# Kernel optimization log

Hardware: AMD Instinct MI355X
Metric: run time of the kernel (lower is better)

The kernel has to match this reference:

```python
import math
import jax, jax.numpy as jnp
import numpy as np

B, L, D, H = 4, 4096, 1024, 16
DK = D // H


def setup_inputs() -> dict:
    key = jax.random.key(0)
    ks = jax.random.split(key, 11)
    s = 0.02
    return {
        "queries": jax.random.normal(ks[0], (B, L, D), jnp.float32),
        "keys": jax.random.normal(ks[1], (B, L, D), jnp.float32),
        "values": jax.random.normal(ks[2], (B, L, D), jnp.float32),
        "Wq": jax.random.normal(ks[3], (D, D), jnp.float32) * s,
        "bq": jnp.zeros((D,), jnp.float32),
        "Wk": jax.random.normal(ks[4], (D, D), jnp.float32) * s,
        "bk": jnp.zeros((D,), jnp.float32),
        "Wv": jax.random.normal(ks[5], (D, D), jnp.float32) * s,
        "bv": jnp.zeros((D,), jnp.float32),
        "Wo": jax.random.normal(ks[6], (D, D), jnp.float32) * s,
        "bo": jnp.zeros((D,), jnp.float32),
    }


def reference(queries, keys, values, Wq, bq, Wk, bk, Wv, bv, Wo, bo):
    # projections + split heads: (B, H, L, DK)
    q = (queries @ Wq + bq).reshape(B, L, H, DK).transpose(0, 2, 1, 3)
    k = (keys @ Wk + bk).reshape(B, L, H, DK).transpose(0, 2, 1, 3)
    v = (values @ Wv + bv).reshape(B, L, H, DK).transpose(0, 2, 1, 3)

    # per-head mean over channel dim -> (B, H, L)
    qm = q.mean(axis=-1)
    km = k.mean(axis=-1)

    # FFT-based autocorrelation: corr (B, H, L)
    qf = jnp.fft.rfft(qm, axis=-1)
    kf = jnp.fft.rfft(km, axis=-1)
    corr = jnp.fft.irfft(qf * jnp.conj(kf), n=L, axis=-1)

    top_k = max(1, int(math.log(L)))  # top_k=None path -> 8 for L=4096
    w, delays = jax.lax.top_k(corr, top_k)          # (B, H, K)
    w = jax.nn.softmax(w, axis=-1)

    # torch.roll(x, shift=d): out[i] = x[(i - d) mod L]
    pos = jnp.arange(L)
    out = jnp.zeros_like(v)
    for kk in range(top_k):
        idx = (pos[None, None, :] - delays[:, :, kk, None]) % L  # (B, H, L)
        rolled = jnp.take_along_axis(v, idx[..., None], axis=2)  # (B, H, L, DK)
        out = out + w[:, :, kk, None, None] * rolled

    # merge heads (matches per-head concat order) and output projection
    out = out.transpose(0, 2, 1, 3).reshape(B, L, D)
    return out @ Wo + bo
```

## Files before the change

kernel.cpp:

```cpp
#include <hip/hip_runtime.h>
#include <hip/hip_bf16.h>
#include <cstdint>

#define BB 4
#define LL 4096
#define DD 1024
#define HH 16
#define DKH 64
#define MROWS 16384
#define KTOP 8
#define RPB 16

typedef float f32x4 __attribute__((ext_vector_type(4)));
typedef _Float16 f16;
typedef _Float16 f16x4 __attribute__((ext_vector_type(4)));
typedef _Float16 f16x8 __attribute__((ext_vector_type(8)));

__device__ __forceinline__ void gll16(const void* g, void* l) {
    __builtin_amdgcn_global_load_lds(
        (const __attribute__((address_space(1))) void*)g,
        (__attribute__((address_space(3))) void*)l, 16, 0, 0);
}

template <int CTRL>
__device__ __forceinline__ float dppf(float x) {
    return __builtin_bit_cast(float,
        __builtin_amdgcn_update_dpp(0, __builtin_bit_cast(int, x), CTRL, 0xF, 0xF, true));
}

__global__ void k_colmeans(const float* __restrict__ Wq, const float* __restrict__ bq,
                           const float* __restrict__ Wk, const float* __restrict__ bk,
                           float* __restrict__ Wqm_t, float* __restrict__ Wkm_t,
                           float* __restrict__ bqm, float* __restrict__ bkm) {
    int t = blockIdx.x * blockDim.x + threadIdx.x;
    int which = t >> 14;
    int idx = t & 16383;
    int d = idx >> 4;
    int h = idx & 15;
    const float* W = which ? Wk : Wq;
    const float* p = W + d * DD + h * DKH;
    float s = 0.f;
    #pragma unroll
    for (int c = 0; c < DKH; ++c) s += p[c];
    (which ? Wkm_t : Wqm_t)[h * DD + d] = s * (1.0f / DKH);
    if (d == 0) {
        const float* bb = which ? bk : bq;
        float sb = 0.f;
        for (int c = 0; c < DKH; ++c) sb += bb[h * DKH + c];
        (which ? bkm : bqm)[h] = sb * (1.0f / DKH);
    }
}

__global__ void k_transpose_cvt(const float* __restrict__ in, f16* __restrict__ out) {
    __shared__ float tile[32][33];
    int k0 = blockIdx.x * 32;
    int n0 = blockIdx.y * 32;
    int tx = threadIdx.x, ty = threadIdx.y;
    #pragma unroll
    for (int j = 0; j < 32; j += 8)
        tile[ty + j][tx] = in[(k0 + ty + j) * DD + n0 + tx];
    __syncthreads();
    #pragma unroll
    for (int j = 0; j < 32; j += 8)
        out[(n0 + ty + j) * DD + k0 + tx] = (f16)tile[tx][ty + j];
}

__global__ void k_cvt_f16(const float* __restrict__ in, f16* __restrict__ out) {
    int i = blockIdx.x * blockDim.x + threadIdx.x;
    f32x4 v = ((const f32x4*)in)[i];
    f16x4 o;
    o[0] = (f16)v.x; o[1] = (f16)v.y; o[2] = (f16)v.z; o[3] = (f16)v.w;
    ((f16x4*)out)[i] = o;
}

__global__ __launch_bounds__(256, 4) void k_means(const float* __restrict__ q, const float* __restrict__ k,
                        const float* __restrict__ Wqm_t, const float* __restrict__ Wkm_t,
                        const float* __restrict__ bqm, const float* __restrict__ bkm,
                        float* __restrict__ qm, float* __restrict__ km) {
    __shared__ float lred[RPB * 264];
    int isK = blockIdx.x & 1;
    int rb  = blockIdx.x >> 1;
    const float* src = isK ? k : q;
    const float* W   = isK ? Wkm_t : Wqm_t;
    const float* bm  = isK ? bkm : bqm;
    float* dst = isK ? km : qm;
    int t = threadIdx.x;
    int wavei = t >> 6, lane = t & 63;
    int c = wavei * 256 + lane * 4;
    f32x4 wr[16];
    #pragma unroll
    for (int h = 0; h < 16; ++h) wr[h] = *(const f32x4*)(W + h * DD + c);
    #pragma unroll
    for (int h = 0; h < 16; ++h) asm volatile("" : "+v"(wr[h]));
    const float* rbase = src + (size_t)rb * RPB * DD + c;
    f32x4 rv = *(const f32x4*)rbase;
    #pragma unroll
    for (int r = 0; r < RPB; ++r) {
        f32x4 nxt = rv;
        if (r + 1 < RPB) nxt = *(const f32x4*)(rbase + (r + 1) * DD);
        float v[16];
        #pragma unroll
        for (int h = 0; h < 16; ++h)
            v[h] = rv.x * wr[h].x + rv.y * wr[h].y + rv.z * wr[h].z + rv.w * wr[h].w;
        float u[8];
        #pragma unroll
        for (int i = 0; i < 8; ++i) {
            float keep = (lane & 1) ? v[2*i+1] : v[2*i];
            float send = (lane & 1) ? v[2*i]   : v[2*i+1];
            u[i] = keep + dppf<0xB1>(send);
        }
        float w2[4];
        #pragma unroll
        for (int i = 0; i < 4; ++i) {
            float keep = (lane & 2) ? u[2*i+1] : u[2*i];
            float send = (lane & 2) ? u[2*i]   : u[2*i+1];
            w2[i] = keep + dppf<0x4E>(send);
        }
        float y[2];
        #pragma unroll
        for (int i = 0; i < 2; ++i) {
            float keep = (lane & 8) ? w2[2*i+1] : w2[2*i];
            float send = (lane & 8) ? w2[2*i]   : w2[2*i+1];
            y[i] = keep + dppf<0x128>(send);
        }
        {
            float keep = (lane & 4) ? y[1] : y[0];
            float send = (lane & 4) ? y[0] : y[1];
            float z = keep + __shfl_xor(send, 4);
            lred[r * 264 + wavei * 64 + lane] = z;
        }
        rv = nxt;
    }
    __syncthreads();
    int rr = t >> 4, h = t & 15;
    int lp = (h & 3) | (((h >> 2) & 1) << 3) | (((h >> 3) & 1) << 2);
    float s = bm[h];
    #pragma unroll
    for (int w = 0; w < 4; ++w)
        #pragma unroll
        for (int g = 0; g < 4; ++g)
            s += lred[rr * 264 + w * 64 + g * 16 + lp];
    int row = rb * RPB + rr;
    int b = row >> 12, l = row & 4095;
    dst[((size_t)((b << 4) + h) << 12) + l] = s;
}

__global__ __launch_bounds__(1024) void k_corr(const float* __restrict__ qm,
                                               const float* __restrict__ km,
                                               float* __restrict__ corr) {
    __shared__ float sq[LL];
    __shared__ f32x4 red[1024];
    int bh = blockIdx.x >> 2;
    int lag0 = (blockIdx.x & 3) * 1024;
    const f32x4* qg = (const f32x4*)(qm + bh * LL);
    const f32x4* kg = (const f32x4*)(km + bh * LL);
    f32x4* sq4 = (f32x4*)sq;
    int t = threadIdx.x;
    for (int i = t; i < LL / 4; i += 1024) sq4[i] = qg[i];
    __syncthreads();
    int lt = t & 255;
    int ms = t >> 8;
    int d0 = lag0 + lt * 4;
    int m0 = ms * 1024;
    float a0 = 0, a1 = 0, a2 = 0, a3 = 0;
    f32x4 wv = sq4[((m0 + d0) & 4095) >> 2];
    float w0 = wv.x, w1 = wv.y, w2 = wv.z, w3 = wv.w;
    #pragma unroll 4
    for (int m = m0; m < m0 + 1024; m += 4) {
        f32x4 nx = sq4[((m + 4 + d0) & 4095) >> 2];
        int mi = __builtin_amdgcn_readfirstlane(m >> 2);
        f32x4 kv = kg[mi];
        a0 += kv.x * w0;  a1 += kv.x * w1;  a2 += kv.x * w2;  a3 += kv.x * w3;
        a0 += kv.y * w1;  a1 += kv.y * w2;  a2 += kv.y * w3;  a3 += kv.y * nx.x;
        a0 += kv.z * w2;  a1 += kv.z * w3;  a2 += kv.z * nx.x; a3 += kv.z * nx.y;
        a0 += kv.w * w3;  a1 += kv.w * nx.x; a2 += kv.w * nx.y; a3 += kv.w * nx.z;
        w0 = nx.x; w1 = nx.y; w2 = nx.z; w3 = nx.w;
    }
    f32x4 p; p.x = a0; p.y = a1; p.z = a2; p.w = a3;
    red[t] = p;
    __syncthreads();
    if (t < 256) {
        f32x4 s0 = red[t], s1 = red[256 + t], s2 = red[512 + t], s3 = red[768 + t];
        f32x4 s;
        s.x = s0.x + s1.x + s2.x + s3.x;
        s.y = s0.y + s1.y + s2.y + s3.y;
        s.z = s0.z + s1.z + s2.z + s3.z;
        s.w = s0.w + s1.w + s2.w + s3.w;
        *(f32x4*)(corr + bh * LL + lag0 + t * 4) = s;
    }
}

__global__ __launch_bounds__(256) void k_topk(const float* __restrict__ corr,
                                              float* __restrict__ wts, int* __restrict__ dls) {
    __shared__ float sc[LL];
    __shared__ float rv[4]; __shared__ int ri[4];
    __shared__ float topv[KTOP]; __shared__ int topi[KTOP];
    int bh = blockIdx.x;
    for (int i = threadIdx.x; i < LL; i += 256) sc[i] = corr[bh * LL + i];
    for (int kk = 0; kk < KTOP; ++kk) {
        __syncthreads();
        float bv = -1e30f; int bi = 0;
        for (int i = threadIdx.x; i < LL; i += 256) {
            float v = sc[i];
            if (v > bv) { bv = v; bi = i; }
        }
        #pragma unroll
        for (int off = 32; off; off >>= 1) {
            float ov = __shfl_down(bv, off);
            int oi = __shfl_down(bi, off);
            if (ov > bv || (ov == bv && oi < bi)) { bv = ov; bi = oi; }
        }
        int wid = threadIdx.x >> 6;
        if ((threadIdx.x & 63) == 0) { rv[wid] = bv; ri[wid] = bi; }
        __syncthreads();
        if (threadIdx.x == 0) {
            for (int w = 1; w < 4; ++w)
                if (rv[w] > bv || (rv[w] == bv && ri[w] < bi)) { bv = rv[w]; bi = ri[w]; }
            topv[kk] = bv; topi[kk] = bi;
            sc[bi] = -1e30f;
        }
    }
    __syncthreads();
    if (threadIdx.x == 0) {
        float mx = topv[0], s = 0.f, e[KTOP];
        #pragma unroll
        for (int kk = 0; kk < KTOP; ++kk) { e[kk] = __expf(topv[kk] - mx); s += e[kk]; }
        float inv = 1.0f / s;
        #pragma unroll
        for (int kk = 0; kk < KTOP; ++kk) {
            wts[bh * KTOP + kk] = e[kk] * inv;
            dls[bh * KTOP + kk] = topi[kk];
        }
    }
}

#define BM 128
#define BN 128
#define BKK 32
template <int MODE>
__global__ __launch_bounds__(256) void k_gemm_bt(const f16* __restrict__ A,
                                                 const f16* __restrict__ BT,
                                                 const float* __restrict__ bias,
                                                 void* __restrict__ Cout) {
    __shared__ f16 As[2][BM * BKK];
    __shared__ f16 Bs[2][BN * BKK];
    const int K = DD;
    int m0 = blockIdx.x * BM;
    int n0 = blockIdx.y * BN;
    int tid = threadIdx.x;
    int lane = tid & 63;
    int wave = tid >> 6;
    int wm = wave & 1, wn = wave >> 1;

    int row0 = tid >> 2;
    int slot = tid & 3;
    int kc0 = slot ^ ((row0 >> 1) & 3);
    int row1 = row0 + 64;
    int kc1 = slot ^ ((row1 >> 1) & 3);
    const f16* gA0 = A + (size_t)(m0 + row0) * K + kc0 * 8;
    const f16* gA1 = A + (size_t)(m0 + row1) * K + kc1 * 8;
    const f16* gB0 = BT + (size_t)(n0 + row0) * K + kc0 * 8;
    const f16* gB1 = BT + (size_t)(n0 + row1) * K + kc1 * 8;

    int fr = lane & 15;
    int quad = lane >> 4;
    int a_off[4], b_off[4];
    #pragma unroll
    for (int i = 0; i < 4; ++i) {
        int ra = wm * 64 + i * 16 + fr;
        a_off[i] = (ra * 4 + (quad ^ ((ra >> 1) & 3))) * 8;
        int rb = wn * 64 + i * 16 + fr;
        b_off[i] = (rb * 4 + (quad ^ ((rb >> 1) & 3))) * 8;
    }

    f32x4 acc[4][4] = {};

    auto STAGE = [&](int b) {
        char* la = (char*)As + b * 8192 + wave * 1024;
        char* lb = (char*)Bs + b * 8192 + wave * 1024;
        gll16(gA0, la);
        gll16(gA1, la + 4096);
        gll16(gB0, lb);
        gll16(gB1, lb + 4096);
        gA0 += BKK; gA1 += BKK; gB0 += BKK; gB1 += BKK;
    };
    auto COMPUTE = [&](int b) {
        const f16* Ab = As[b];
        const f16* Bb = Bs[b];
        f16x8 af[4], bf[4];
        #pragma unroll
        for (int i = 0; i < 4; ++i) af[i] = *(const f16x8*)(Ab + a_off[i]);
        #pragma unroll
        for (int i = 0; i < 4; ++i) bf[i] = *(const f16x8*)(Bb + b_off[i]);
        #pragma unroll
        for (int im = 0; im < 4; ++im)
            #pragma unroll
            for (int in = 0; in < 4; ++in)
                acc[im][in] = __builtin_amdgcn_mfma_f32_16x16x32_f16(af[im], bf[in], acc[im][in], 0, 0, 0);
    };

    STAGE(0);
    __syncthreads();
    const int NT = K / BKK;
    for (int kt = 0; kt < NT - 1; ++kt) {
        STAGE((kt & 1) ^ 1);
        COMPUTE(kt & 1);
        __syncthreads();
    }
    COMPUTE((NT - 1) & 1);

    #pragma unroll
    for (int in = 0; in < 4; ++in) {
        int col = n0 + wn * 64 + in * 16 + fr;
        float bb = bias[col];
        #pragma unroll
        for (int im = 0; im < 4; ++im) {
            int rowb = m0 + wm * 64 + im * 16 + quad * 4;
            #pragma unroll
            for (int r = 0; r < 4; ++r) {
                float val = acc[im][in][r] + bb;
                if (MODE == 0) {
                    int rr = rowb + r;
                    int b = rr >> 12, l = rr & 4095, h = col >> 6, c = col & 63;
                    ((f16*)Cout)[((size_t)(((b << 4) + h) << 12) + l) * 64 + c] = (f16)val;
                } else {
                    ((float*)Cout)[(size_t)(rowb + r) * DD + col] = val;
                }
            }
        }
    }
}

__global__ __launch_bounds__(256) void k_roll(const f16* __restrict__ V,
                                              const float* __restrict__ wts,
                                              const int* __restrict__ dls,
                                              f16* __restrict__ out) {
    int x = blockIdx.x;
    int wk = ((x & 7) << 10) | (x >> 3);
    int t = wk * 256 + threadIdx.x;
    int cc = t & 7;
    int l = (t >> 3) & 4095;
    int bh = t >> 15;
    const f16* vb = V + ((size_t)bh << 18);
    float a[8] = {};
    #pragma unroll
    for (int kk = 0; kk < KTOP; ++kk) {
        float w = wts[bh * KTOP + kk];
        int d = dls[bh * KTOP + kk];
        int src = (l - d) & 4095;
        f16x8 vv = *(const f16x8*)(vb + (src << 6) + (cc << 3));
        #pragma unroll
        for (int j = 0; j < 8; ++j) a[j] += w * (float)vv[j];
    }
    f16* o = out + ((size_t)((bh >> 4) << 12) + l) * 1024 + ((bh & 15) << 6) + (cc << 3);
    f16x8 ov;
    #pragma unroll
    for (int j = 0; j < 8; ++j) ov[j] = (f16)a[j];
    *(f16x8*)o = ov;
}

extern "C" void kernel_launch(void* const* d_in, const int* in_sizes, int n_in,
                              void* d_out, int out_size, void* d_ws, size_t ws_size,
                              hipStream_t stream) {
    const float* queries = (const float*)d_in[0];
    const float* keys    = (const float*)d_in[1];
    const float* values  = (const float*)d_in[2];
    const float* Wq = (const float*)d_in[3];
    const float* bq = (const float*)d_in[4];
    const float* Wk = (const float*)d_in[5];
    const float* bk = (const float*)d_in[6];
    const float* Wv = (const float*)d_in[7];
    const float* bv = (const float*)d_in[8];
    const float* Wo = (const float*)d_in[9];
    const float* bo = (const float*)d_in[10];

    char* ws = (char*)d_ws;
    size_t off = 0;
    auto alloc = [&](size_t bytes) -> char* {
        char* p = ws + off;
        off += (bytes + 255) & ~(size_t)255;
        return p;
    };
    f16*   values_f16 = (f16*)alloc((size_t)MROWS * DD * 2);
    f16*   Vbuf       = (f16*)alloc((size_t)MROWS * DD * 2);
    f16*   WvT        = (f16*)alloc((size_t)DD * DD * 2);
    f16*   WoT        = (f16*)alloc((size_t)DD * DD * 2);
    float* Wqm_t      = (float*)alloc(HH * DD * 4);
    float* Wkm_t      = (float*)alloc(HH * DD * 4);
    float* bqm        = (float*)alloc(HH * 4);
    float* bkm        = (float*)alloc(HH * 4);
    float* qm         = (float*)alloc((size_t)BB * HH * LL * 4);
    float* km         = (float*)alloc((size_t)BB * HH * LL * 4);
    float* corr       = (float*)alloc((size_t)BB * HH * LL * 4);
    float* wts        = (float*)alloc(BB * HH * KTOP * 4);
    int*   dls        = (int*)alloc(BB * HH * KTOP * 4);
    f16*   out_f16    = values_f16;

    k_colmeans<<<128, 256, 0, stream>>>(Wq, bq, Wk, bk, Wqm_t, Wkm_t, bqm, bkm);
    k_transpose_cvt<<<dim3(32, 32), dim3(32, 8), 0, stream>>>(Wv, WvT);
    k_transpose_cvt<<<dim3(32, 32), dim3(32, 8), 0, stream>>>(Wo, WoT);
    k_cvt_f16<<<16384, 256, 0, stream>>>(values, values_f16);
    k_means<<<2048, 256, 0, stream>>>(queries, keys, Wqm_t, Wkm_t, bqm, bkm, qm, km);
    k_corr<<<256, 1024, 0, stream>>>(qm, km, corr);
    k_topk<<<64, 256, 0, stream>>>(corr, wts, dls);
    k_gemm_bt<0><<<dim3(MROWS / BM, DD / BN), 256, 0, stream>>>(values_f16, WvT, bv, Vbuf);
    k_roll<<<8192, 256, 0, stream>>>(Vbuf, wts, dls, out_f16);
    k_gemm_bt<1><<<dim3(MROWS / BM, DD / BN), 256, 0, stream>>>(out_f16, WoT, bo, d_out);
}
```

Baseline: 449.0 us.

## Triple-buffer GEMM LDS tiles with explicit vmcnt waits and raw barriers

Expands the GEMM shared-memory staging from two to three buffers so two K-tiles are in flight while one is computed. The loop is unrolled by three, with `s_waitcnt vmcnt(4)` plus `s_barrier` replacing `__syncthreads`. Only the current tile's async global-to-LDS loads are awaited, which keeps more memory latency hidden behind MFMA work. In exchange, LDS per block rises to 48KB, which can lower occupancy, and correctness now depends on hand-counted outstanding loads.

```diff
diff --git a/kernel.cpp b/kernel.cpp
--- a/kernel.cpp
+++ b/kernel.cpp
@@ -242,8 +242,8 @@
                                                  const f16* __restrict__ BT,
                                                  const float* __restrict__ bias,
                                                  void* __restrict__ Cout) {
-    __shared__ f16 As[2][BM * BKK];
-    __shared__ f16 Bs[2][BN * BKK];
+    __shared__ f16 As[3][BM * BKK];
+    __shared__ f16 Bs[3][BN * BKK];
     const int K = DD;
     int m0 = blockIdx.x * BM;
     int n0 = blockIdx.y * BN;
@@ -275,18 +275,18 @@
 
     f32x4 acc[4][4] = {};
 
-    auto STAGE = [&](int b) {
-        char* la = (char*)As + b * 8192 + wave * 1024;
-        char* lb = (char*)Bs + b * 8192 + wave * 1024;
-        gll16(gA0, la);
-        gll16(gA1, la + 4096);
-        gll16(gB0, lb);
-        gll16(gB1, lb + 4096);
-        gA0 += BKK; gA1 += BKK; gB0 += BKK; gB1 += BKK;
+    auto STAGE = [&](int b, int kt) {
+        char* la = (char*)(&As[b][0]) + wave * 1024;
+        char* lb = (char*)(&Bs[b][0]) + wave * 1024;
+        int ko = kt * BKK;
+        gll16(gA0 + ko, la);
+        gll16(gA1 + ko, la + 4096);
+        gll16(gB0 + ko, lb);
+        gll16(gB1 + ko, lb + 4096);
     };
     auto COMPUTE = [&](int b) {
-        const f16* Ab = As[b];
-        const f16* Bb = Bs[b];
+        const f16* Ab = &As[b][0];
+        const f16* Bb = &Bs[b][0];
         f16x8 af[4], bf[4];
         #pragma unroll
         for (int i = 0; i < 4; ++i) af[i] = *(const f16x8*)(Ab + a_off[i]);
@@ -299,15 +299,29 @@
                 acc[im][in] = __builtin_amdgcn_mfma_f32_16x16x32_f16(af[im], bf[in], acc[im][in], 0, 0, 0);
     };
 
-    STAGE(0);
-    __syncthreads();
     const int NT = K / BKK;
-    for (int kt = 0; kt < NT - 1; ++kt) {
-        STAGE((kt & 1) ^ 1);
-        COMPUTE(kt & 1);
-        __syncthreads();
-    }
-    COMPUTE((NT - 1) & 1);
+    STAGE(0, 0);
+    STAGE(1, 1);
+    for (int ii = 0; ii < NT - 2; ii += 3) {
+        asm volatile("s_waitcnt vmcnt(4)" ::: "memory");
+        __builtin_amdgcn_s_barrier();
+        STAGE(2, ii + 2);
+        COMPUTE(0);
+        asm volatile("s_waitcnt vmcnt(4)" ::: "memory");
+        __builtin_amdgcn_s_barrier();
+        STAGE(0, ii + 3);
+        COMPUTE(1);
+        asm volatile("s_waitcnt vmcnt(4)" ::: "memory");
+        __builtin_amdgcn_s_barrier();
+        STAGE(1, ii + 4);
+        COMPUTE(2);
+    }
+    asm volatile("s_waitcnt vmcnt(4)" ::: "memory");
+    __builtin_amdgcn_s_barrier();
+    COMPUTE(0);
+    asm volatile("s_waitcnt vmcnt(0)" ::: "memory");
+    __builtin_amdgcn_s_barrier();
+    COMPUTE(1);
 
     #pragma unroll
     for (int in = 0; in < 4; ++in) {
```

New measurement: 437.2 us. 2.6% less time.

## Enlarge GEMM M-tile, load B fragments directly from global, widen corr key loads

Applied to the files above, without the earlier changes.

The GEMM now uses a 256x128 tile. B operand fragments are loaded straight from global memory into registers instead of being staged through LDS, so LDS holds only the A tile. The main loop is unrolled by two with explicit register double-buffering. The correlation kernel loads 16 keys per wavefront-uniform load with one-group prefetch, cutting the number of scalar loads. This should improve MFMA arithmetic intensity and halve LDS traffic per FLOP, but it raises register pressure and relies on uncoalesced per-lane global loads for B.

```diff
diff --git a/kernel.cpp b/kernel.cpp
--- a/kernel.cpp
+++ b/kernel.cpp
@@ -12,6 +12,7 @@
 #define RPB 16
 
 typedef float f32x4 __attribute__((ext_vector_type(4)));
+typedef float f32x16 __attribute__((ext_vector_type(16)));
 typedef _Float16 f16;
 typedef _Float16 f16x4 __attribute__((ext_vector_type(4)));
 typedef _Float16 f16x8 __attribute__((ext_vector_type(8)));
@@ -153,7 +154,7 @@
     int bh = blockIdx.x >> 2;
     int lag0 = (blockIdx.x & 3) * 1024;
     const f32x4* qg = (const f32x4*)(qm + bh * LL);
-    const f32x4* kg = (const f32x4*)(km + bh * LL);
+    const f32x16* kg16 = (const f32x16*)(km + bh * LL);
     f32x4* sq4 = (f32x4*)sq;
     int t = threadIdx.x;
     for (int i = t; i < LL / 4; i += 1024) sq4[i] = qg[i];
@@ -162,19 +163,26 @@
     int ms = t >> 8;
     int d0 = lag0 + lt * 4;
     int m0 = ms * 1024;
+    int gi0 = m0 >> 4;
     float a0 = 0, a1 = 0, a2 = 0, a3 = 0;
     f32x4 wv = sq4[((m0 + d0) & 4095) >> 2];
     float w0 = wv.x, w1 = wv.y, w2 = wv.z, w3 = wv.w;
-    #pragma unroll 4
-    for (int m = m0; m < m0 + 1024; m += 4) {
-        f32x4 nx = sq4[((m + 4 + d0) & 4095) >> 2];
-        int mi = __builtin_amdgcn_readfirstlane(m >> 2);
-        f32x4 kv = kg[mi];
-        a0 += kv.x * w0;  a1 += kv.x * w1;  a2 += kv.x * w2;  a3 += kv.x * w3;
-        a0 += kv.y * w1;  a1 += kv.y * w2;  a2 += kv.y * w3;  a3 += kv.y * nx.x;
-        a0 += kv.z * w2;  a1 += kv.z * w3;  a2 += kv.z * nx.x; a3 += kv.z * nx.y;
-        a0 += kv.w * w3;  a1 += kv.w * nx.x; a2 += kv.w * nx.y; a3 += kv.w * nx.z;
-        w0 = nx.x; w1 = nx.y; w2 = nx.z; w3 = nx.w;
+    f32x16 kv = kg16[__builtin_amdgcn_readfirstlane(gi0)];
+    for (int g = 0; g < 64; ++g) {
+        f32x16 kvn = kv;
+        if (g < 63) kvn = kg16[__builtin_amdgcn_readfirstlane(gi0 + g + 1)];
+        #pragma unroll
+        for (int j = 0; j < 4; ++j) {
+            int m = m0 + g * 16 + j * 4;
+            f32x4 nx = sq4[((m + 4 + d0) & 4095) >> 2];
+            float kx = kv[4*j+0], ky = kv[4*j+1], kz = kv[4*j+2], kw = kv[4*j+3];
+            a0 += kx * w0;  a1 += kx * w1;  a2 += kx * w2;  a3 += kx * w3;
+            a0 += ky * w1;  a1 += ky * w2;  a2 += ky * w3;  a3 += ky * nx.x;
+            a0 += kz * w2;  a1 += kz * w3;  a2 += kz * nx.x; a3 += kz * nx.y;
+            a0 += kw * w3;  a1 += kw * nx.x; a2 += kw * nx.y; a3 += kw * nx.z;
+            w0 = nx.x; w1 = nx.y; w2 = nx.z; w3 = nx.w;
+        }
+        kv = kvn;
     }
     f32x4 p; p.x = a0; p.y = a1; p.z = a2; p.w = a3;
     red[t] = p;
@@ -234,16 +242,15 @@
     }
 }
 
-#define BM 128
+#define BM 256
 #define BN 128
 #define BKK 32
 template <int MODE>
-__global__ __launch_bounds__(256) void k_gemm_bt(const f16* __restrict__ A,
-                                                 const f16* __restrict__ BT,
-                                                 const float* __restrict__ bias,
-                                                 void* __restrict__ Cout) {
+__global__ __launch_bounds__(256, 2) void k_gemm_bt(const f16* __restrict__ A,
+                                                    const f16* __restrict__ BT,
+                                                    const float* __restrict__ bias,
+                                                    void* __restrict__ Cout) {
     __shared__ f16 As[2][BM * BKK];
-    __shared__ f16 Bs[2][BN * BKK];
     const int K = DD;
     int m0 = blockIdx.x * BM;
     int n0 = blockIdx.y * BN;
@@ -252,70 +259,82 @@
     int wave = tid >> 6;
     int wm = wave & 1, wn = wave >> 1;
 
-    int row0 = tid >> 2;
+    int rowS = tid >> 2;
     int slot = tid & 3;
-    int kc0 = slot ^ ((row0 >> 1) & 3);
-    int row1 = row0 + 64;
-    int kc1 = slot ^ ((row1 >> 1) & 3);
-    const f16* gA0 = A + (size_t)(m0 + row0) * K + kc0 * 8;
-    const f16* gA1 = A + (size_t)(m0 + row1) * K + kc1 * 8;
-    const f16* gB0 = BT + (size_t)(n0 + row0) * K + kc0 * 8;
-    const f16* gB1 = BT + (size_t)(n0 + row1) * K + kc1 * 8;
+    int kcS = slot ^ ((rowS >> 1) & 3);
+    const f16* gA0 = A + (size_t)(m0 + rowS) * K + kcS * 8;
+    const f16* gA1 = A + (size_t)(m0 + rowS + 64) * K + kcS * 8;
+    const f16* gA2 = A + (size_t)(m0 + rowS + 128) * K + kcS * 8;
+    const f16* gA3 = A + (size_t)(m0 + rowS + 192) * K + kcS * 8;
 
     int fr = lane & 15;
     int quad = lane >> 4;
-    int a_off[4], b_off[4];
-    #pragma unroll
-    for (int i = 0; i < 4; ++i) {
-        int ra = wm * 64 + i * 16 + fr;
+    int a_off[8];
+    #pragma unroll
+    for (int i = 0; i < 8; ++i) {
+        int ra = wm * 128 + i * 16 + fr;
         a_off[i] = (ra * 4 + (quad ^ ((ra >> 1) & 3))) * 8;
-        int rb = wn * 64 + i * 16 + fr;
-        b_off[i] = (rb * 4 + (quad ^ ((rb >> 1) & 3))) * 8;
-    }
-
-    f32x4 acc[4][4] = {};
-
-    auto STAGE = [&](int b) {
-        char* la = (char*)As + b * 8192 + wave * 1024;
-        char* lb = (char*)Bs + b * 8192 + wave * 1024;
-        gll16(gA0, la);
-        gll16(gA1, la + 4096);
-        gll16(gB0, lb);
-        gll16(gB1, lb + 4096);
-        gA0 += BKK; gA1 += BKK; gB0 += BKK; gB1 += BKK;
+    }
+    const f16* gB[4];
+    #pragma unroll
+    for (int i = 0; i < 4; ++i)
+        gB[i] = BT + (size_t)(n0 + wn * 64 + i * 16 + fr) * K + quad * 8;
+
+    f32x4 acc[8][4] = {};
+    f16x8 b0[4], b1[4];
+
+    auto STAGE = [&](int buf, int kt) {
+        char* la = (char*)(&As[buf][0]) + wave * 1024;
+        int ko = kt * BKK;
+        gll16(gA0 + ko, la);
+        gll16(gA1 + ko, la + 4096);
+        gll16(gA2 + ko, la + 8192);
+        gll16(gA3 + ko, la + 12288);
     };
-    auto COMPUTE = [&](int b) {
-        const f16* Ab = As[b];
-        const f16* Bb = Bs[b];
-        f16x8 af[4], bf[4];
-        #pragma unroll
-        for (int i = 0; i < 4; ++i) af[i] = *(const f16x8*)(Ab + a_off[i]);
-        #pragma unroll
-        for (int i = 0; i < 4; ++i) bf[i] = *(const f16x8*)(Bb + b_off[i]);
-        #pragma unroll
-        for (int im = 0; im < 4; ++im)
+    auto LOADB = [&](f16x8 (&bd)[4], int kt) {
+        int ko = kt * BKK;
+        #pragma unroll
+        for (int i = 0; i < 4; ++i) bd[i] = *(const f16x8*)(gB[i] + ko);
+    };
+    auto COMPUTE = [&](int buf, f16x8 (&bc)[4]) {
+        const f16* Ab = &As[buf][0];
+        f16x8 af[8];
+        #pragma unroll
+        for (int i = 0; i < 8; ++i) af[i] = *(const f16x8*)(Ab + a_off[i]);
+        #pragma unroll
+        for (int im = 0; im < 8; ++im)
             #pragma unroll
             for (int in = 0; in < 4; ++in)
-                acc[im][in] = __builtin_amdgcn_mfma_f32_16x16x32_f16(af[im], bf[in], acc[im][in], 0, 0, 0);
+                acc[im][in] = __builtin_amdgcn_mfma_f32_16x16x32_f16(af[im], bc[in], acc[im][in], 0, 0, 0);
     };
 
-    STAGE(0);
-    __syncthreads();
     const int NT = K / BKK;
-    for (int kt = 0; kt < NT - 1; ++kt) {
-        STAGE((kt & 1) ^ 1);
-        COMPUTE(kt & 1);
+    STAGE(0, 0);
+    LOADB(b0, 0);
+    __syncthreads();
+    for (int kt = 0; kt < NT - 2; kt += 2) {
+        STAGE(1, kt + 1);
+        LOADB(b1, kt + 1);
+        COMPUTE(0, b0);
         __syncthreads();
-    }
-    COMPUTE((NT - 1) & 1);
+        STAGE(0, kt + 2);
+        LOADB(b0, kt + 2);
+        COMPUTE(1, b1);
+        __syncthreads();
+    }
+    STAGE(1, NT - 1);
+    LOADB(b1, NT - 1);
+    COMPUTE(0, b0);
+    __syncthreads();
+    COMPUTE(1, b1);
 
     #pragma unroll
     for (int in = 0; in < 4; ++in) {
         int col = n0 + wn * 64 + in * 16 + fr;
         float bb = bias[col];
         #pragma unroll
-        for (int im = 0; im < 4; ++im) {
-            int rowb = m0 + wm * 64 + im * 16 + quad * 4;
+        for (int im = 0; im < 8; ++im) {
+            int rowb = m0 + wm * 128 + im * 16 + quad * 4;
             #pragma unroll
             for (int r = 0; r < 4; ++r) {
                 float val = acc[im][in][r] + bb;
```

Result: faster. 434.4 us (-3.3%).
